# Kernel tuning notes

Measured on AMD Instinct MI355X. Metric: run time of the kernel, lower is better.

Reference implementation:

```python
import jax, jax.numpy as jnp
import numpy as np

K_PRED = 6
SCORE_TEMPERATURE = 0.5
NMS_THRESH = np.array([2.5, 1.0, 1.5], dtype=np.float32)  # [veh, ped, cyc] meters
SUPPRESSED_SCORE = 0.001


def setup_inputs() -> dict:
    key = jax.random.key(0)
    k0, k1, k2, k3 = jax.random.split(key, 4)
    D, S, A, P, T = 1, 64, 128, 6, 80  # n_decoder, n_scene, n_agent, n_pred, n_step_future
    pred_valid = jnp.ones((S, A), dtype=bool)
    pred_conf = jax.random.normal(k0, (D, S, A, P), dtype=jnp.float32)
    # scale positions to realistic meters so distances straddle the NMS thresholds
    pred_pos = jax.random.normal(k1, (D, S, A, P, T, 2), dtype=jnp.float32) * 10.0
    pred_yaw_bbox = jax.random.normal(k2, (D, S, A, P, T, 1), dtype=jnp.float32)
    type_idx = jax.random.randint(k3, (S, A), 0, 3)
    ref_type = jax.nn.one_hot(type_idx, 3, dtype=jnp.float32)
    return {
        'pred_valid': pred_valid,
        'pred_conf': pred_conf,
        'pred_pos': pred_pos,
        'pred_yaw_bbox': pred_yaw_bbox,
        'ref_type': ref_type,
    }


def _nms_one_agent(scores, within, valid):
    # scores: [K], within: [K, K] bool, valid: scalar bool
    order = jnp.argsort(-scores)  # descending, computed once on original scores

    def step(cur, k):
        # suppress k if any other prediction within distance has a (currently) higher score
        mask = within[k] & (cur > cur[k])
        new_val = jnp.where(jnp.any(mask), jnp.asarray(SUPPRESSED_SCORE, cur.dtype), cur[k])
        return cur.at[k].set(new_val), None

    out, _ = jax.lax.scan(step, scores, order)
    return jnp.where(valid, out, scores)


_nms = jax.vmap(jax.vmap(_nms_one_agent))  # over scene, agent


def reference(pred_valid, pred_conf, pred_pos, pred_yaw_bbox, ref_type):
    D, S, A, P, T, _ = pred_pos.shape
    K = D * P
    # [n_scene, n_agent, k_pred, n_step, 2]
    trajs = jnp.moveaxis(pred_pos, 0, 2).reshape(S, A, K, T, 2)
    scores = jax.nn.softmax(pred_conf, axis=-1)
    scores = jnp.moveaxis(scores, 0, 2).reshape(S, A, K)
    scores = scores / jnp.sum(scores, axis=-1, keepdims=True)

    # mpa_nms: per-agent-type distance threshold
    thresh = jnp.einsum('sat,t->sa', ref_type, jnp.asarray(NMS_THRESH))[:, :, None, None]
    # use_ade=True: mean pairwise distance over time -> [S, A, K, K]
    diff = trajs[:, :, :, None] - trajs[:, :, None, :]          # [S,A,K,K,T,2]
    within_dist = jnp.mean(jnp.linalg.norm(diff, axis=-1), axis=-1) < thresh
    scores = _nms(scores, within_dist, pred_valid)
    scores = scores / jnp.sum(scores, axis=-1, keepdims=True)

    # score temperature
    scores = jax.nn.softmax(jnp.log(scores) / SCORE_TEMPERATURE, axis=-1)

    waymo_trajs = jnp.moveaxis(trajs, 3, 1)                      # [S, T, A, K, 2]
    waymo_scores = scores                                        # [S, A, K]
    waymo_valid = jnp.broadcast_to(pred_valid[:, None, :], (S, T, A))
    yaw_bbox = jnp.moveaxis(pred_yaw_bbox, 0, 2).reshape(S, A, K, T, 1)
    waymo_yaw_bbox = jnp.moveaxis(yaw_bbox, 3, 1)                # [S, T, A, K, 1]
    return waymo_valid, waymo_trajs, waymo_scores, waymo_yaw_bbox
```

## Files before the change

### kernel.cpp

```cpp
#include <hip/hip_runtime.h>
#include <hip/hip_bf16.h>

#define NS 64
#define NA 128
#define NK 6
#define NT 80
#define TILE_A 8
#define THREADS 256

#define OFF_TRAJ   655360
#define OFF_SCORE  (655360 + 7864320)
#define OFF_YAW    (655360 + 7864320 + 49152)

__global__ __launch_bounds__(THREADS) void waymo_post_kernel(
    const int*    __restrict__ validIn,
    const float*  __restrict__ confIn,
    const float2* __restrict__ posIn,
    const float*  __restrict__ yawIn,
    const float*  __restrict__ typeIn,
    float*        __restrict__ out)
{
    const int s   = blockIdx.y;
    const int a0  = blockIdx.x * TILE_A;
    const int tid = threadIdx.x;

    __shared__ float2 sPos[TILE_A * NK * 81];
    __shared__ float  sYaw[TILE_A * NK * 81];

    const size_t base = ((size_t)(s * NA + a0)) * NK * NT;
    for (int i = tid; i < TILE_A * NK * NT; i += THREADS) {
        int r = i / NT;
        int t = i - r * NT;
        sPos[r * 81 + t] = posIn[base + i];
        sYaw[r * 81 + t] = yawIn[base + i];
    }
    __syncthreads();

    float*  outV  = out;
    float2* outT  = (float2*)(out + OFF_TRAJ);
    float*  outSc = out + OFF_SCORE;
    float*  outY  = out + OFF_YAW;

    {
        const int la   = tid >> 5;
        const int lane = tid & 31;
        const int a    = a0 + la;
        const int p    = lane >> 1;
        const int half = lane & 1;

        const size_t sa = (size_t)s * NA + a;
        const float th = 2.5f * typeIn[sa * 3 + 0]
                       + 1.0f * typeIn[sa * 3 + 1]
                       + 1.5f * typeIn[sa * 3 + 2];

        int pi, pj;
        if      (p < 5)  { pi = 0; pj = p + 1; }
        else if (p < 9)  { pi = 1; pj = p - 3; }
        else if (p < 12) { pi = 2; pj = p - 6; }
        else if (p < 14) { pi = 3; pj = p - 8; }
        else             { pi = 4; pj = 5;     }

        const int rI = la * NK + pi, rJ = la * NK + pj;
        float dsum = 0.f;
        for (int t = half * 40; t < half * 40 + 40; ++t) {
            float2 u = sPos[rI * 81 + t];
            float2 v = sPos[rJ * 81 + t];
            float dx = u.x - v.x, dy = u.y - v.y;
            dsum += sqrtf(dx * dx + dy * dy);
        }
        dsum += __shfl_xor(dsum, 1);
        const bool within = (dsum / 80.0f) < th;
        const bool predb  = (half == 0) && (p < 15) && within;
        unsigned long long bal = __ballot(predb);
        unsigned mask32 = (unsigned)(bal >> (tid & 32));

        if (lane == 0) {
            float c[NK];
            float mx = -3e38f;
            for (int q = 0; q < NK; ++q) { c[q] = confIn[sa * NK + q]; mx = fmaxf(mx, c[q]); }
            float ssum = 0.f;
            for (int q = 0; q < NK; ++q) { c[q] = expf(c[q] - mx); ssum += c[q]; }
            for (int q = 0; q < NK; ++q) c[q] /= ssum;
            ssum = 0.f;
            for (int q = 0; q < NK; ++q) ssum += c[q];
            for (int q = 0; q < NK; ++q) c[q] /= ssum;

            int ord[NK]; bool used[NK];
            for (int q = 0; q < NK; ++q) used[q] = false;
            for (int st = 0; st < NK; ++st) {
                int best = 0; float bv = -3e38f;
                for (int q = 0; q < NK; ++q)
                    if (!used[q] && c[q] > bv) { bv = c[q]; best = q; }
                used[best] = true; ord[st] = best;
            }

            float cur[NK];
            for (int q = 0; q < NK; ++q) cur[q] = c[q];

            if (validIn[sa] != 0) {
                for (int st = 0; st < NK; ++st) {
                    int k = ord[st];
                    float ck = cur[k];
                    bool any = false;
                    for (int j = 0; j < NK; ++j) {
                        if (j == k) continue;
                        int lo = j < k ? j : k;
                        int hi = j < k ? k : j;
                        int pidx = lo * 5 - (lo * (lo - 1)) / 2 + (hi - lo - 1);
                        if (((mask32 >> (2 * pidx)) & 1u) && (cur[j] > ck)) any = true;
                    }
                    if (any) cur[k] = 0.001f;
                }
            }

            float tsum = 0.f;
            for (int q = 0; q < NK; ++q) tsum += cur[q];
            float w[NK]; float wsum = 0.f;
            for (int q = 0; q < NK; ++q) {
                float qq = cur[q] / tsum;
                w[q] = qq * qq; wsum += w[q];
            }
            for (int q = 0; q < NK; ++q) outSc[sa * NK + q] = w[q] / wsum;
        }
    }

    for (int o = tid; o < TILE_A * NK * NT; o += THREADS) {
        int t  = o / (TILE_A * NK);
        int r  = o - t * (TILE_A * NK);
        int la = r / NK;
        int k  = r - la * NK;
        size_t oidx = ((size_t)(s * NT + t) * NA + (a0 + la)) * NK + k;
        outT[oidx] = sPos[r * 81 + t];
        outY[oidx] = sYaw[r * 81 + t];
    }

    for (int o = tid; o < NT * TILE_A; o += THREADS) {
        int t  = o >> 3;
        int la = o & 7;
        outV[(size_t)(s * NT + t) * NA + a0 + la] =
            (validIn[(size_t)s * NA + a0 + la] != 0) ? 1.0f : 0.0f;
    }
}

extern "C" void kernel_launch(void* const* d_in, const int* in_sizes, int n_in,
                              void* d_out, int out_size, void* d_ws, size_t ws_size,
                              hipStream_t stream) {
    const int*    validIn = (const int*)d_in[0];
    const float*  confIn  = (const float*)d_in[1];
    const float2* posIn   = (const float2*)d_in[2];
    const float*  yawIn   = (const float*)d_in[3];
    const float*  typeIn  = (const float*)d_in[4];
    float* out = (float*)d_out;

    dim3 grid(NA / TILE_A, NS);
    waymo_post_kernel<<<grid, THREADS, 0, stream>>>(validIn, confIn, posIn, yawIn, typeIn, out);
}
```

Baseline: 42.50 us.

## Split kernel into interleaved transpose-copy blocks and NMS score blocks

Replaces the single per-(scene, 8-agent) block with a 1D grid that interleaves two block kinds. Five of every six blocks transpose a 16-timestep tile of positions and yaw into the output layout, using nontemporal stores. Every sixth block computes the pairwise ADE distances directly from global memory and runs the per-agent NMS and score normalisation. The aim is more blocks and smaller shared-memory tiles for better occupancy and bandwidth on the copy path. In exchange, the score blocks re-read positions from global memory without shared-memory staging.

```diff
diff --git a/kernel.cpp b/kernel.cpp
--- a/kernel.cpp
+++ b/kernel.cpp
@@ -5,12 +5,20 @@
 #define NA 128
 #define NK 6
 #define NT 80
+#define THREADS 256
+
 #define TILE_A 8
-#define THREADS 256
+#define TILE_T 16
+#define NROWS (TILE_A * NK)
+#define N_TT (NT / TILE_T)
+#define NBT (NS * (NA / TILE_A) * N_TT)
+#define NBS (NS * (NA / TILE_A))
 
 #define OFF_TRAJ   655360
 #define OFF_SCORE  (655360 + 7864320)
 #define OFF_YAW    (655360 + 7864320 + 49152)
+
+typedef float nfloat2 __attribute__((ext_vector_type(2)));
 
 __global__ __launch_bounds__(THREADS) void waymo_post_kernel(
     const int*    __restrict__ validIn,
@@ -20,28 +28,58 @@
     const float*  __restrict__ typeIn,
     float*        __restrict__ out)
 {
-    const int s   = blockIdx.y;
-    const int a0  = blockIdx.x * TILE_A;
+    const int g   = blockIdx.x;
     const int tid = threadIdx.x;
-
-    __shared__ float2 sPos[TILE_A * NK * 81];
-    __shared__ float  sYaw[TILE_A * NK * 81];
-
-    const size_t base = ((size_t)(s * NA + a0)) * NK * NT;
-    for (int i = tid; i < TILE_A * NK * NT; i += THREADS) {
-        int r = i / NT;
-        int t = i - r * NT;
-        sPos[r * 81 + t] = posIn[base + i];
-        sYaw[r * 81 + t] = yawIn[base + i];
-    }
-    __syncthreads();
 
     float*  outV  = out;
     float2* outT  = (float2*)(out + OFF_TRAJ);
     float*  outSc = out + OFF_SCORE;
     float*  outY  = out + OFF_YAW;
 
-    {
+    __shared__ float2 sPos[NROWS * 17];
+    __shared__ float  sYaw[NROWS * 17];
+
+    if ((g % 6) != 0) {
+        const int tb  = g - (g / 6 + 1);
+        const int s   = tb / ((NA / TILE_A) * N_TT);
+        const int rem = tb % ((NA / TILE_A) * N_TT);
+        const int at  = rem / N_TT;
+        const int tt  = rem % N_TT;
+        const int a0  = at * TILE_A;
+        const int t0  = tt * TILE_T;
+
+        const size_t base = ((size_t)(s * NA + a0)) * NK * NT;
+
+        for (int i = tid; i < NROWS * TILE_T; i += THREADS) {
+            int r = i >> 4;
+            int t = i & (TILE_T - 1);
+            sPos[r * 17 + t] = posIn[base + (size_t)r * NT + t0 + t];
+            sYaw[r * 17 + t] = yawIn[base + (size_t)r * NT + t0 + t];
+        }
+        __syncthreads();
+
+        for (int o = tid; o < NROWS * TILE_T; o += THREADS) {
+            int t = o / NROWS;
+            int r = o - t * NROWS;
+            int la = r / NK;
+            int k  = r - la * NK;
+            size_t oidx = ((size_t)(s * NT + t0 + t) * NA + (a0 + la)) * NK + k;
+            float2 pv = sPos[r * 17 + t];
+            __builtin_nontemporal_store(*(nfloat2*)&pv, (nfloat2*)&outT[oidx]);
+            __builtin_nontemporal_store(sYaw[r * 17 + t], &outY[oidx]);
+        }
+
+        for (int o = tid; o < TILE_T * TILE_A; o += THREADS) {
+            int t  = o >> 3;
+            int la = o & 7;
+            float v = (validIn[(size_t)s * NA + a0 + la] != 0) ? 1.0f : 0.0f;
+            __builtin_nontemporal_store(v, &outV[(size_t)(s * NT + t0 + t) * NA + a0 + la]);
+        }
+    } else {
+        const int sb = g / 6;
+        const int s  = sb / (NA / TILE_A);
+        const int a0 = (sb % (NA / TILE_A)) * TILE_A;
+
         const int la   = tid >> 5;
         const int lane = tid & 31;
         const int a    = a0 + la;
@@ -60,11 +98,12 @@
         else if (p < 14) { pi = 3; pj = p - 8; }
         else             { pi = 4; pj = 5;     }
 
-        const int rI = la * NK + pi, rJ = la * NK + pj;
+        const float2* row = posIn + sa * (NK * NT);
         float dsum = 0.f;
+        #pragma unroll 8
         for (int t = half * 40; t < half * 40 + 40; ++t) {
-            float2 u = sPos[rI * 81 + t];
-            float2 v = sPos[rJ * 81 + t];
+            float2 u = row[pi * NT + t];
+            float2 v = row[pj * NT + t];
             float dx = u.x - v.x, dy = u.y - v.y;
             dsum += sqrtf(dx * dx + dy * dy);
         }
@@ -123,23 +162,6 @@
             for (int q = 0; q < NK; ++q) outSc[sa * NK + q] = w[q] / wsum;
         }
     }
-
-    for (int o = tid; o < TILE_A * NK * NT; o += THREADS) {
-        int t  = o / (TILE_A * NK);
-        int r  = o - t * (TILE_A * NK);
-        int la = r / NK;
-        int k  = r - la * NK;
-        size_t oidx = ((size_t)(s * NT + t) * NA + (a0 + la)) * NK + k;
-        outT[oidx] = sPos[r * 81 + t];
-        outY[oidx] = sYaw[r * 81 + t];
-    }
-
-    for (int o = tid; o < NT * TILE_A; o += THREADS) {
-        int t  = o >> 3;
-        int la = o & 7;
-        outV[(size_t)(s * NT + t) * NA + a0 + la] =
-            (validIn[(size_t)s * NA + a0 + la] != 0) ? 1.0f : 0.0f;
-    }
 }
 
 extern "C" void kernel_launch(void* const* d_in, const int* in_sizes, int n_in,
@@ -152,6 +174,5 @@
     const float*  typeIn  = (const float*)d_in[4];
     float* out = (float*)d_out;
 
-    dim3 grid(NA / TILE_A, NS);
-    waymo_post_kernel<<<grid, THREADS, 0, stream>>>(validIn, confIn, posIn, yawIn, typeIn, out);
+    waymo_post_kernel<<<NBT + NBS, THREADS, 0, stream>>>(validIn, confIn, posIn, yawIn, typeIn, out);
 }
```

Result: slower. 55.88 us (+31.5%).

## Split into vectorized transpose kernel and separate NMS score kernel

Applied to the files above, without the earlier changes.

The fused kernel is split in two. A transpose kernel tiles over agent and time, loads with 16-byte vector reads, and writes the trajectory, yaw and valid outputs with vectorized nontemporal stores. A separate score kernel reloads positions to compute the pairwise ADE masks and the NMS scores. This targets the scattered, poorly coalesced output stores of the original, at the cost of a second launch and reading the position data twice.

```diff
diff --git a/kernel.cpp b/kernel.cpp
--- a/kernel.cpp
+++ b/kernel.cpp
@@ -5,140 +5,187 @@
 #define NA 128
 #define NK 6
 #define NT 80
-#define TILE_A 8
-#define THREADS 256
 
 #define OFF_TRAJ   655360
 #define OFF_SCORE  (655360 + 7864320)
 #define OFF_YAW    (655360 + 7864320 + 49152)
 
-__global__ __launch_bounds__(THREADS) void waymo_post_kernel(
+typedef float nfloat4 __attribute__((ext_vector_type(4)));
+
+#define TA 16
+#define TT 16
+#define RT (TA * NK)
+
+__global__ __launch_bounds__(256) void waymo_transpose_kernel(
+    const int*    __restrict__ validIn,
+    const float2* __restrict__ posIn,
+    const float*  __restrict__ yawIn,
+    float*        __restrict__ out)
+{
+    const int g   = blockIdx.x;
+    const int tid = threadIdx.x;
+    const int s   = g / 40;
+    const int rem = g - s * 40;
+    const int a0  = (rem / 5) * TA;
+    const int t0  = (rem - (rem / 5) * 5) * TT;
+
+    __shared__ float2 sT[TT][RT + 1];
+    __shared__ float  yT[TT][RT + 1];
+
+    const size_t sa0 = (size_t)s * NA + a0;
+    const float2* pbase = posIn + sa0 * (NK * NT);
+    const float*  ybase = yawIn + sa0 * (NK * NT);
+
+    for (int i = tid; i < RT * 8; i += 256) {
+        int r = i >> 3, l = i & 7;
+        nfloat4 v = *(const nfloat4*)(pbase + (size_t)r * NT + t0 + 2 * l);
+        sT[2 * l + 0][r] = float2{v.x, v.y};
+        sT[2 * l + 1][r] = float2{v.z, v.w};
+    }
+    for (int i = tid; i < RT * 4; i += 256) {
+        int r = i >> 2, m = i & 3;
+        nfloat4 v = *(const nfloat4*)(ybase + (size_t)r * NT + t0 + 4 * m);
+        yT[4 * m + 0][r] = v.x;
+        yT[4 * m + 1][r] = v.y;
+        yT[4 * m + 2][r] = v.z;
+        yT[4 * m + 3][r] = v.w;
+    }
+    __syncthreads();
+
+    nfloat4* trajOut = (nfloat4*)(out + OFF_TRAJ);
+    for (int o = tid; o < TT * 48; o += 256) {
+        int t = o / 48, j = o - (o / 48) * 48;
+        size_t f4 = (((size_t)(s * NT + t0 + t) * NA + a0) * NK) >> 1;
+        float2 u = sT[t][2 * j], w = sT[t][2 * j + 1];
+        nfloat4 v{u.x, u.y, w.x, w.y};
+        __builtin_nontemporal_store(v, trajOut + f4 + j);
+    }
+    nfloat4* yawOut = (nfloat4*)(out + OFF_YAW);
+    for (int o = tid; o < TT * 24; o += 256) {
+        int t = o / 24, j = o - (o / 24) * 24;
+        size_t f4 = (((size_t)(s * NT + t0 + t) * NA + a0) * NK) >> 2;
+        nfloat4 v{yT[t][4 * j], yT[t][4 * j + 1], yT[t][4 * j + 2], yT[t][4 * j + 3]};
+        __builtin_nontemporal_store(v, yawOut + f4 + j);
+    }
+    if (tid < 64) {
+        int t = tid >> 2, q = tid & 3;
+        nfloat4 v;
+        v.x = (validIn[sa0 + 4 * q + 0] != 0) ? 1.0f : 0.0f;
+        v.y = (validIn[sa0 + 4 * q + 1] != 0) ? 1.0f : 0.0f;
+        v.z = (validIn[sa0 + 4 * q + 2] != 0) ? 1.0f : 0.0f;
+        v.w = (validIn[sa0 + 4 * q + 3] != 0) ? 1.0f : 0.0f;
+        size_t f4 = ((size_t)(s * NT + t0 + t) * NA + a0) >> 2;
+        __builtin_nontemporal_store(v, (nfloat4*)out + f4 + q);
+    }
+}
+
+#define SA8 8
+
+__global__ __launch_bounds__(256) void waymo_score_kernel(
     const int*    __restrict__ validIn,
     const float*  __restrict__ confIn,
     const float2* __restrict__ posIn,
-    const float*  __restrict__ yawIn,
     const float*  __restrict__ typeIn,
     float*        __restrict__ out)
 {
-    const int s   = blockIdx.y;
-    const int a0  = blockIdx.x * TILE_A;
+    const int g   = blockIdx.x;
     const int tid = threadIdx.x;
-
-    __shared__ float2 sPos[TILE_A * NK * 81];
-    __shared__ float  sYaw[TILE_A * NK * 81];
-
-    const size_t base = ((size_t)(s * NA + a0)) * NK * NT;
-    for (int i = tid; i < TILE_A * NK * NT; i += THREADS) {
-        int r = i / NT;
-        int t = i - r * NT;
-        sPos[r * 81 + t] = posIn[base + i];
-        sYaw[r * 81 + t] = yawIn[base + i];
+    const int s   = g / (NA / SA8);
+    const int a0  = (g - s * (NA / SA8)) * SA8;
+
+    __shared__ float2 sPos[SA8 * NK * 82];
+
+    const size_t sab = (size_t)s * NA + a0;
+    const float2* pbase = posIn + sab * (NK * NT);
+
+    for (int i = tid; i < SA8 * NK * (NT / 2); i += 256) {
+        int r = i / 40, q = i - (i / 40) * 40;
+        nfloat4 v = *(const nfloat4*)(pbase + (size_t)r * NT + 2 * q);
+        *(nfloat4*)&sPos[r * 82 + 2 * q] = v;
     }
     __syncthreads();
 
-    float*  outV  = out;
-    float2* outT  = (float2*)(out + OFF_TRAJ);
-    float*  outSc = out + OFF_SCORE;
-    float*  outY  = out + OFF_YAW;
-
-    {
-        const int la   = tid >> 5;
-        const int lane = tid & 31;
-        const int a    = a0 + la;
-        const int p    = lane >> 1;
-        const int half = lane & 1;
-
-        const size_t sa = (size_t)s * NA + a;
-        const float th = 2.5f * typeIn[sa * 3 + 0]
-                       + 1.0f * typeIn[sa * 3 + 1]
-                       + 1.5f * typeIn[sa * 3 + 2];
-
-        int pi, pj;
-        if      (p < 5)  { pi = 0; pj = p + 1; }
-        else if (p < 9)  { pi = 1; pj = p - 3; }
-        else if (p < 12) { pi = 2; pj = p - 6; }
-        else if (p < 14) { pi = 3; pj = p - 8; }
-        else             { pi = 4; pj = 5;     }
-
-        const int rI = la * NK + pi, rJ = la * NK + pj;
-        float dsum = 0.f;
-        for (int t = half * 40; t < half * 40 + 40; ++t) {
-            float2 u = sPos[rI * 81 + t];
-            float2 v = sPos[rJ * 81 + t];
-            float dx = u.x - v.x, dy = u.y - v.y;
-            dsum += sqrtf(dx * dx + dy * dy);
+    float* outSc = out + OFF_SCORE;
+
+    const int la   = tid >> 5;
+    const int lane = tid & 31;
+    const int a    = a0 + la;
+    const int p    = lane >> 1;
+    const int half = lane & 1;
+
+    const size_t sa = (size_t)s * NA + a;
+    const float th = 2.5f * typeIn[sa * 3 + 0]
+                   + 1.0f * typeIn[sa * 3 + 1]
+                   + 1.5f * typeIn[sa * 3 + 2];
+
+    int pi, pj;
+    if      (p < 5)  { pi = 0; pj = p + 1; }
+    else if (p < 9)  { pi = 1; pj = p - 3; }
+    else if (p < 12) { pi = 2; pj = p - 6; }
+    else if (p < 14) { pi = 3; pj = p - 8; }
+    else             { pi = 4; pj = 5;     }
+
+    const int rI = la * NK + pi, rJ = la * NK + pj;
+    float dsum = 0.f;
+    for (int t = half * 40; t < half * 40 + 40; ++t) {
+        float2 u = sPos[rI * 82 + t];
+        float2 v = sPos[rJ * 82 + t];
+        float dx = u.x - v.x, dy = u.y - v.y;
+        dsum += sqrtf(dx * dx + dy * dy);
+    }
+    dsum += __shfl_xor(dsum, 1);
+    const bool within = (dsum / 80.0f) < th;
+    const bool predb  = (half == 0) && (p < 15) && within;
+    unsigned long long bal = __ballot(predb);
+    unsigned mask32 = (unsigned)(bal >> (tid & 32));
+
+    if (lane == 0) {
+        float c[NK];
+        float mx = -3e38f;
+        for (int q = 0; q < NK; ++q) { c[q] = confIn[sa * NK + q]; mx = fmaxf(mx, c[q]); }
+        float ssum = 0.f;
+        for (int q = 0; q < NK; ++q) { c[q] = expf(c[q] - mx); ssum += c[q]; }
+        for (int q = 0; q < NK; ++q) c[q] /= ssum;
+        ssum = 0.f;
+        for (int q = 0; q < NK; ++q) ssum += c[q];
+        for (int q = 0; q < NK; ++q) c[q] /= ssum;
+
+        int ord[NK]; bool used[NK];
+        for (int q = 0; q < NK; ++q) used[q] = false;
+        for (int st = 0; st < NK; ++st) {
+            int best = 0; float bv = -3e38f;
+            for (int q = 0; q < NK; ++q)
+                if (!used[q] && c[q] > bv) { bv = c[q]; best = q; }
+            used[best] = true; ord[st] = best;
         }
-        dsum += __shfl_xor(dsum, 1);
-        const bool within = (dsum / 80.0f) < th;
-        const bool predb  = (half == 0) && (p < 15) && within;
-        unsigned long long bal = __ballot(predb);
-        unsigned mask32 = (unsigned)(bal >> (tid & 32));
-
-        if (lane == 0) {
-            float c[NK];
-            float mx = -3e38f;
-            for (int q = 0; q < NK; ++q) { c[q] = confIn[sa * NK + q]; mx = fmaxf(mx, c[q]); }
-            float ssum = 0.f;
-            for (int q = 0; q < NK; ++q) { c[q] = expf(c[q] - mx); ssum += c[q]; }
-            for (int q = 0; q < NK; ++q) c[q] /= ssum;
-            ssum = 0.f;
-            for (int q = 0; q < NK; ++q) ssum += c[q];
-            for (int q = 0; q < NK; ++q) c[q] /= ssum;
-
-            int ord[NK]; bool used[NK];
-            for (int q = 0; q < NK; ++q) used[q] = false;
+
+        float cur[NK];
+        for (int q = 0; q < NK; ++q) cur[q] = c[q];
+
+        if (validIn[sa] != 0) {
             for (int st = 0; st < NK; ++st) {
-                int best = 0; float bv = -3e38f;
-                for (int q = 0; q < NK; ++q)
-                    if (!used[q] && c[q] > bv) { bv = c[q]; best = q; }
-                used[best] = true; ord[st] = best;
+                int k = ord[st];
+                float ck = cur[k];
+                bool any = false;
+                for (int j = 0; j < NK; ++j) {
+                    if (j == k) continue;
+                    int lo = j < k ? j : k;
+                    int hi = j < k ? k : j;
+                    int pidx = lo * 5 - (lo * (lo - 1)) / 2 + (hi - lo - 1);
+                    if (((mask32 >> (2 * pidx)) & 1u) && (cur[j] > ck)) any = true;
+                }
+                if (any) cur[k] = 0.001f;
             }
-
-            float cur[NK];
-            for (int q = 0; q < NK; ++q) cur[q] = c[q];
-
-            if (validIn[sa] != 0) {
-                for (int st = 0; st < NK; ++st) {
-                    int k = ord[st];
-                    float ck = cur[k];
-                    bool any = false;
-                    for (int j = 0; j < NK; ++j) {
-                        if (j == k) continue;
-                        int lo = j < k ? j : k;
-                        int hi = j < k ? k : j;
-                        int pidx = lo * 5 - (lo * (lo - 1)) / 2 + (hi - lo - 1);
-                        if (((mask32 >> (2 * pidx)) & 1u) && (cur[j] > ck)) any = true;
-                    }
-                    if (any) cur[k] = 0.001f;
-                }
-            }
-
-            float tsum = 0.f;
-            for (int q = 0; q < NK; ++q) tsum += cur[q];
-            float w[NK]; float wsum = 0.f;
-            for (int q = 0; q < NK; ++q) {
-                float qq = cur[q] / tsum;
-                w[q] = qq * qq; wsum += w[q];
-            }
-            for (int q = 0; q < NK; ++q) outSc[sa * NK + q] = w[q] / wsum;
         }
-    }
-
-    for (int o = tid; o < TILE_A * NK * NT; o += THREADS) {
-        int t  = o / (TILE_A * NK);
-        int r  = o - t * (TILE_A * NK);
-        int la = r / NK;
-        int k  = r - la * NK;
-        size_t oidx = ((size_t)(s * NT + t) * NA + (a0 + la)) * NK + k;
-        outT[oidx] = sPos[r * 81 + t];
-        outY[oidx] = sYaw[r * 81 + t];
-    }
-
-    for (int o = tid; o < NT * TILE_A; o += THREADS) {
-        int t  = o >> 3;
-        int la = o & 7;
-        outV[(size_t)(s * NT + t) * NA + a0 + la] =
-            (validIn[(size_t)s * NA + a0 + la] != 0) ? 1.0f : 0.0f;
+
+        float tsum = 0.f;
+        for (int q = 0; q < NK; ++q) tsum += cur[q];
+        float w[NK]; float wsum = 0.f;
+        for (int q = 0; q < NK; ++q) {
+            float qq = cur[q] / tsum;
+            w[q] = qq * qq; wsum += w[q];
+        }
+        for (int q = 0; q < NK; ++q) outSc[sa * NK + q] = w[q] / wsum;
     }
 }
 
@@ -152,6 +199,6 @@
     const float*  typeIn  = (const float*)d_in[4];
     float* out = (float*)d_out;
 
-    dim3 grid(NA / TILE_A, NS);
-    waymo_post_kernel<<<grid, THREADS, 0, stream>>>(validIn, confIn, posIn, yawIn, typeIn, out);
+    waymo_transpose_kernel<<<NS * 8 * 5, 256, 0, stream>>>(validIn, posIn, yawIn, out);
+    waymo_score_kernel<<<NS * (NA / SA8), 256, 0, stream>>>(validIn, confIn, posIn, typeIn, out);
 }
```

Result: slower. 46.43 us (+9.2%).

## Vectorize global loads and transposed stores with float4 and nontemporal writes

Applied to the files above, without the earlier changes.

Loads of positions and yaw into shared memory now use 16-byte vector loads, with padded row strides chosen for alignment. The transposed output writes for trajectories, yaw and the valid mask become float4 nontemporal stores instead of scalar or float2 stores. The block grows to 512 threads, with only the first 256 doing the NMS work, and the grid is flattened to one dimension. The goal is fewer, wider memory transactions in this bandwidth-bound kernel. The costs are more shared-memory padding, possible LDS bank conflicts in the gather, and idle threads during the NMS phase.

```diff
diff --git a/kernel.cpp b/kernel.cpp
--- a/kernel.cpp
+++ b/kernel.cpp
@@ -5,12 +5,18 @@
 #define NA 128
 #define NK 6
 #define NT 80
+#define THREADS 512
 #define TILE_A 8
-#define THREADS 256
+#define NROWS (TILE_A * NK)
 
 #define OFF_TRAJ   655360
 #define OFF_SCORE  (655360 + 7864320)
 #define OFF_YAW    (655360 + 7864320 + 49152)
+
+#define PSTRIDE 82
+#define YSTRIDE 84
+
+typedef float nfloat4 __attribute__((ext_vector_type(4)));
 
 __global__ __launch_bounds__(THREADS) void waymo_post_kernel(
     const int*    __restrict__ validIn,
@@ -20,28 +26,33 @@
     const float*  __restrict__ typeIn,
     float*        __restrict__ out)
 {
-    const int s   = blockIdx.y;
-    const int a0  = blockIdx.x * TILE_A;
+    const int g   = blockIdx.x;
     const int tid = threadIdx.x;
+    const int s   = g >> 4;
+    const int a0  = (g & 15) * TILE_A;
 
-    __shared__ float2 sPos[TILE_A * NK * 81];
-    __shared__ float  sYaw[TILE_A * NK * 81];
+    __shared__ float2 sPos[NROWS * PSTRIDE];
+    __shared__ float  sYaw[NROWS * YSTRIDE];
 
-    const size_t base = ((size_t)(s * NA + a0)) * NK * NT;
-    for (int i = tid; i < TILE_A * NK * NT; i += THREADS) {
-        int r = i / NT;
-        int t = i - r * NT;
-        sPos[r * 81 + t] = posIn[base + i];
-        sYaw[r * 81 + t] = yawIn[base + i];
+    const size_t sa0 = (size_t)s * NA + a0;
+    const float2* pbase = posIn + sa0 * (NK * NT);
+    const float*  ybase = yawIn + sa0 * (NK * NT);
+
+    for (int i = tid; i < NROWS * (NT / 2); i += THREADS) {
+        int r = i / 40, q = i - r * 40;
+        nfloat4 v = *(const nfloat4*)(pbase + (size_t)r * NT + 2 * q);
+        *(nfloat4*)&sPos[r * PSTRIDE + 2 * q] = v;
+    }
+    for (int i = tid; i < NROWS * (NT / 4); i += THREADS) {
+        int r = i / 20, m = i - r * 20;
+        nfloat4 v = *(const nfloat4*)(ybase + (size_t)r * NT + 4 * m);
+        *(nfloat4*)&sYaw[r * YSTRIDE + 4 * m] = v;
     }
     __syncthreads();
 
-    float*  outV  = out;
-    float2* outT  = (float2*)(out + OFF_TRAJ);
-    float*  outSc = out + OFF_SCORE;
-    float*  outY  = out + OFF_YAW;
+    float* outSc = out + OFF_SCORE;
 
-    {
+    if (tid < 256) {
         const int la   = tid >> 5;
         const int lane = tid & 31;
         const int a    = a0 + la;
@@ -63,8 +74,8 @@
         const int rI = la * NK + pi, rJ = la * NK + pj;
         float dsum = 0.f;
         for (int t = half * 40; t < half * 40 + 40; ++t) {
-            float2 u = sPos[rI * 81 + t];
-            float2 v = sPos[rJ * 81 + t];
+            float2 u = sPos[rI * PSTRIDE + t];
+            float2 v = sPos[rJ * PSTRIDE + t];
             float dx = u.x - v.x, dy = u.y - v.y;
             dsum += sqrtf(dx * dx + dy * dy);
         }
@@ -124,21 +135,34 @@
         }
     }
 
-    for (int o = tid; o < TILE_A * NK * NT; o += THREADS) {
-        int t  = o / (TILE_A * NK);
-        int r  = o - t * (TILE_A * NK);
-        int la = r / NK;
-        int k  = r - la * NK;
-        size_t oidx = ((size_t)(s * NT + t) * NA + (a0 + la)) * NK + k;
-        outT[oidx] = sPos[r * 81 + t];
-        outY[oidx] = sYaw[r * 81 + t];
+    nfloat4* trajOut = (nfloat4*)(out + OFF_TRAJ);
+    for (int o = tid; o < NT * 24; o += THREADS) {
+        int t = o / 24, j = o - (o / 24) * 24;
+        float2 u = sPos[(2 * j + 0) * PSTRIDE + t];
+        float2 w = sPos[(2 * j + 1) * PSTRIDE + t];
+        nfloat4 v{u.x, u.y, w.x, w.y};
+        size_t f4 = (((size_t)(s * NT + t) * NA + a0) * NK) >> 1;
+        __builtin_nontemporal_store(v, trajOut + f4 + j);
     }
-
-    for (int o = tid; o < NT * TILE_A; o += THREADS) {
-        int t  = o >> 3;
-        int la = o & 7;
-        outV[(size_t)(s * NT + t) * NA + a0 + la] =
-            (validIn[(size_t)s * NA + a0 + la] != 0) ? 1.0f : 0.0f;
+    nfloat4* yawOut = (nfloat4*)(out + OFF_YAW);
+    for (int o = tid; o < NT * 12; o += THREADS) {
+        int t = o / 12, j = o - (o / 12) * 12;
+        nfloat4 v{sYaw[(4 * j + 0) * YSTRIDE + t],
+                  sYaw[(4 * j + 1) * YSTRIDE + t],
+                  sYaw[(4 * j + 2) * YSTRIDE + t],
+                  sYaw[(4 * j + 3) * YSTRIDE + t]};
+        size_t f4 = (((size_t)(s * NT + t) * NA + a0) * NK) >> 2;
+        __builtin_nontemporal_store(v, yawOut + f4 + j);
+    }
+    if (tid < 160) {
+        int t = tid >> 1, q = tid & 1;
+        nfloat4 v;
+        v.x = (validIn[sa0 + 4 * q + 0] != 0) ? 1.0f : 0.0f;
+        v.y = (validIn[sa0 + 4 * q + 1] != 0) ? 1.0f : 0.0f;
+        v.z = (validIn[sa0 + 4 * q + 2] != 0) ? 1.0f : 0.0f;
+        v.w = (validIn[sa0 + 4 * q + 3] != 0) ? 1.0f : 0.0f;
+        size_t f4 = ((size_t)(s * NT + t) * NA + a0) >> 2;
+        __builtin_nontemporal_store(v, (nfloat4*)out + f4 + q);
     }
 }
 
@@ -152,6 +176,6 @@
     const float*  typeIn  = (const float*)d_in[4];
     float* out = (float*)d_out;
 
-    dim3 grid(NA / TILE_A, NS);
-    waymo_post_kernel<<<grid, THREADS, 0, stream>>>(validIn, confIn, posIn, yawIn, typeIn, out);
+    waymo_post_kernel<<<NS * (NA / TILE_A), THREADS, 0, stream>>>(
+        validIn, confIn, posIn, yawIn, typeIn, out);
 }
```

Result: faster. 36.64 us (-13.8%).
